# Performance work log

Measured on AMD Instinct MI355X. Metric: run time of the kernel, lower is better.

## Reference

```python
import math
import jax, jax.numpy as jnp
import numpy as np

EMBED_DIM = 512
MAX_LEN = 5000
BATCH = 16
SEQ = 4096


def _make_pe(max_len, embed_dim):
    pos = jnp.arange(max_len, dtype=jnp.float32)[:, None]
    div = jnp.exp(jnp.arange(0, embed_dim, 2, dtype=jnp.float32) * (-math.log(10000.0) / embed_dim))
    pe = jnp.zeros((max_len, embed_dim), dtype=jnp.float32)
    pe = pe.at[:, 0::2].set(jnp.sin(pos * div))
    pe = pe.at[:, 1::2].set(jnp.cos(pos * div))
    return pe[None]  # [1, max_len, embed_dim]


def setup_inputs() -> dict:
    key = jax.random.key(0)
    k1, k2 = jax.random.split(key)
    x = jax.random.normal(k1, (BATCH, SEQ, EMBED_DIM), dtype=jnp.float32)
    pe = _make_pe(MAX_LEN, EMBED_DIM)
    # RZ angles: present in the original module but provably do not affect
    # the PauliZ expectations (diagonal phases + basis-permuting CNOTs).
    param = jax.random.normal(k2, (EMBED_DIM,), dtype=jnp.float32)
    quantum_weight = jnp.full((1,), 0.5, dtype=jnp.float32)
    return {"x": x, "pe": pe, "param": param, "quantum_weight": quantum_weight}


def reference(x, pe, param, quantum_weight):
    # out = x + positional encoding
    out = x + pe[:, : x.shape[1]]  # [B, S, D]
    # Closed form of the RY(out_i)->RZ(param_i)->CNOT-chain circuit:
    #   b'_i = XOR(b_0..b_i)  =>  <Z_i> = prod_{j<=i} cos(out_j)
    # (RZ phases cancel in computational-basis probabilities; param unused.)
    quantum_out = jnp.cumprod(jnp.cos(out), axis=-1)  # [B, S, D]
    w = jax.nn.sigmoid(quantum_weight[0])
    return w * quantum_out + (1.0 - w) * out
```

## Files before the change

### kernel.cpp

```cpp
#include <hip/hip_runtime.h>

constexpr int D = 512;
constexpr int S = 4096;
constexpr int B = 16;
constexpr int ROWS = B * S;
constexpr int WAVES_PER_BLOCK = 4;
constexpr int ROWS_PER_WAVE  = 2;

typedef float fx4 __attribute__((ext_vector_type(4)));

template<int CTRL, int ROW_MASK>
__device__ __forceinline__ float dpp_mul(float x) {
    int t = __builtin_amdgcn_update_dpp(0x3f800000, __float_as_int(x),
                                        CTRL, ROW_MASK, 0xF, false);
    return x * __int_as_float(t);
}
__device__ __forceinline__ float wave_incl_mul_scan(float p) {
    p = dpp_mul<0x111, 0xF>(p);
    p = dpp_mul<0x112, 0xF>(p);
    p = dpp_mul<0x114, 0xF>(p);
    p = dpp_mul<0x118, 0xF>(p);
    p = dpp_mul<0x142, 0xA>(p);
    p = dpp_mul<0x143, 0xC>(p);
    return p;
}
__device__ __forceinline__ float wave_shr1_id(float p) {
    int t = __builtin_amdgcn_update_dpp(0x3f800000, __float_as_int(p),
                                        0x138 , 0xF, 0xF, false);
    return __int_as_float(t);
}

__global__ __launch_bounds__(256) void qpe_kernel(
    const fx4* __restrict__ x4, const float* __restrict__ qw,
    fx4* __restrict__ out4)
{
    const int lane = threadIdx.x & 63;
    const int wid  = threadIdx.x >> 6;
    const int wave = blockIdx.x * WAVES_PER_BLOCK + wid;
    const int row0 = wave * ROWS_PER_WAVE;

    const float w   = 1.0f / (1.0f + __expf(-qw[0]));
    const float omw = 1.0f - w;

    const float NEG_LOG2_10K_OVER_256 = -0.05190512648261503f;
    float div[4];
    #pragma unroll
    for (int j = 0; j < 4; ++j)
        div[j] = exp2f((float)(lane * 4 + j) * NEG_LOG2_10K_OVER_256);

    size_t xb[ROWS_PER_WAVE];
    fx4 xv[ROWS_PER_WAVE][2];
    #pragma unroll
    for (int r = 0; r < ROWS_PER_WAVE; ++r) {
        xb[r] = (size_t)(row0 + r) * (D / 4) + (size_t)lane * 2;
        xv[r][0] = x4[xb[r]];
        xv[r][1] = x4[xb[r] + 1];
    }

    float o[ROWS_PER_WAVE][8], c[ROWS_PER_WAVE][8], p[ROWS_PER_WAVE];
    #pragma unroll
    for (int r = 0; r < ROWS_PER_WAVE; ++r) {
        const float sf = (float)((row0 + r) & (S - 1));
        float xr[8] = { xv[r][0][0], xv[r][0][1], xv[r][0][2], xv[r][0][3],
                        xv[r][1][0], xv[r][1][1], xv[r][1][2], xv[r][1][3] };
        #pragma unroll
        for (int j = 0; j < 4; ++j) {
            const float a = sf * div[j];
            o[r][2 * j]     = xr[2 * j]     + __sinf(a);
            o[r][2 * j + 1] = xr[2 * j + 1] + __cosf(a);
        }
        #pragma unroll
        for (int j = 0; j < 8; ++j) c[r][j] = __cosf(o[r][j]);
        float q = c[r][0];
        #pragma unroll
        for (int j = 1; j < 8; ++j) q *= c[r][j];
        p[r] = q;
    }

    #pragma unroll
    for (int r = 0; r < ROWS_PER_WAVE; ++r) {
        p[r] = wave_incl_mul_scan(p[r]);
        p[r] = wave_shr1_id(p[r]);
    }

    #pragma unroll
    for (int r = 0; r < ROWS_PER_WAVE; ++r) {
        float run = p[r];
        float res[8];
        #pragma unroll
        for (int j = 0; j < 8; ++j) {
            run *= c[r][j];
            res[j] = w * run + omw * o[r][j];
        }
        fx4 s0 = { res[0], res[1], res[2], res[3] };
        fx4 s1 = { res[4], res[5], res[6], res[7] };
        __builtin_nontemporal_store(s0, &out4[xb[r]]);
        __builtin_nontemporal_store(s1, &out4[xb[r] + 1]);
    }
}

extern "C" void kernel_launch(void* const* d_in, const int* in_sizes, int n_in,
                              void* d_out, int out_size, void* d_ws, size_t ws_size,
                              hipStream_t stream) {
    const fx4* x  = (const fx4*)d_in[0];
    const float* qw  = (const float*)d_in[3];
    fx4* out = (fx4*)d_out;

    const int blocks = ROWS / (WAVES_PER_BLOCK * ROWS_PER_WAVE);
    qpe_kernel<<<blocks, WAVES_PER_BLOCK * 64, 0, stream>>>(x, qw, out);
}
```

Before: 55.78 us.

## Process four rows per wave with per-row fused compute and plain stores

Doubles rows per wave so each wave issues four rows of loads up front, and halves the block count. Per-row compute, scan and store are merged into a single loop, which removes the separate phases that held every row's intermediates live. Nontemporal stores become regular stores. A dead zero-initialisation of o is added; it is overwritten and should be optimised away.

```diff
diff --git a/kernel.cpp b/kernel.cpp
--- a/kernel.cpp
+++ b/kernel.cpp
@@ -5,7 +5,7 @@
 constexpr int B = 16;
 constexpr int ROWS = B * S;
 constexpr int WAVES_PER_BLOCK = 4;
-constexpr int ROWS_PER_WAVE  = 2;
+constexpr int ROWS_PER_WAVE  = 4;
 
 typedef float fx4 __attribute__((ext_vector_type(4)));
 
@@ -57,45 +57,44 @@
         xv[r][1] = x4[xb[r] + 1];
     }
 
-    float o[ROWS_PER_WAVE][8], c[ROWS_PER_WAVE][8], p[ROWS_PER_WAVE];
     #pragma unroll
     for (int r = 0; r < ROWS_PER_WAVE; ++r) {
         const float sf = (float)((row0 + r) & (S - 1));
-        float xr[8] = { xv[r][0][0], xv[r][0][1], xv[r][0][2], xv[r][0][3],
-                        xv[r][1][0], xv[r][1][1], xv[r][1][2], xv[r][1][3] };
+        float o[8], c[8];
         #pragma unroll
         for (int j = 0; j < 4; ++j) {
             const float a = sf * div[j];
-            o[r][2 * j]     = xr[2 * j]     + __sinf(a);
-            o[r][2 * j + 1] = xr[2 * j + 1] + __cosf(a);
+            o[2 * j]     = xv[r][0][0] * 0.0f + 0.0f;
+            o[2 * j + 1] = 0.0f;
+        }
+        {
+            float xr[8] = { xv[r][0][0], xv[r][0][1], xv[r][0][2], xv[r][0][3],
+                            xv[r][1][0], xv[r][1][1], xv[r][1][2], xv[r][1][3] };
+            #pragma unroll
+            for (int j = 0; j < 4; ++j) {
+                const float a = sf * div[j];
+                o[2 * j]     = xr[2 * j]     + __sinf(a);
+                o[2 * j + 1] = xr[2 * j + 1] + __cosf(a);
+            }
         }
         #pragma unroll
-        for (int j = 0; j < 8; ++j) c[r][j] = __cosf(o[r][j]);
-        float q = c[r][0];
+        for (int j = 0; j < 8; ++j) c[j] = __cosf(o[j]);
+
+        float p = c[0];
         #pragma unroll
-        for (int j = 1; j < 8; ++j) q *= c[r][j];
-        p[r] = q;
-    }
+        for (int j = 1; j < 8; ++j) p *= c[j];
 
-    #pragma unroll
-    for (int r = 0; r < ROWS_PER_WAVE; ++r) {
-        p[r] = wave_incl_mul_scan(p[r]);
-        p[r] = wave_shr1_id(p[r]);
-    }
+        p = wave_incl_mul_scan(p);
+        p = wave_shr1_id(p);
 
-    #pragma unroll
-    for (int r = 0; r < ROWS_PER_WAVE; ++r) {
-        float run = p[r];
-        float res[8];
+        float run = p, res[8];
         #pragma unroll
         for (int j = 0; j < 8; ++j) {
-            run *= c[r][j];
-            res[j] = w * run + omw * o[r][j];
+            run *= c[j];
+            res[j] = w * run + omw * o[j];
         }
-        fx4 s0 = { res[0], res[1], res[2], res[3] };
-        fx4 s1 = { res[4], res[5], res[6], res[7] };
-        __builtin_nontemporal_store(s0, &out4[xb[r]]);
-        __builtin_nontemporal_store(s1, &out4[xb[r] + 1]);
+        out4[xb[r]]     = (fx4){ res[0], res[1], res[2], res[3] };
+        out4[xb[r] + 1] = (fx4){ res[4], res[5], res[6], res[7] };
     }
 }
 
```

Measured after the change: 44.83 us. -19.6%, faster.
